# Kernel tuning notes

Hardware: AMD Instinct MI355X
Metric: run time of the kernel (lower is better)

## Reference

```python
import jax, jax.numpy as jnp
import numpy as np

B, P_DIM, H_DIM, X_DIM = 4096, 1024, 2048, 1024


def setup_inputs() -> dict:
    key = jax.random.key(0)
    ks = jax.random.split(key, 24)
    def lin_w(k, out_d, in_d):
        bound = 1.0 / np.sqrt(in_d)
        return jax.random.uniform(k, (out_d, in_d), jnp.float32, -bound, bound)
    def lin_b(k, out_d, in_d):
        bound = 1.0 / np.sqrt(in_d)
        return jax.random.uniform(k, (out_d,), jnp.float32, -bound, bound)
    inp = {
        "P": jax.random.normal(ks[0], (B, P_DIM), jnp.float32),
        "hidden": jax.random.normal(ks[1], (B, H_DIM), jnp.float32),
        "cell": jax.random.normal(ks[2], (B, H_DIM), jnp.float32),
        "ext_input": jax.random.normal(ks[3], (B, X_DIM), jnp.float32),
        "W_pi": lin_w(ks[4], H_DIM, P_DIM), "b_pi": lin_b(ks[5], H_DIM, P_DIM),
        "W_pf": lin_w(ks[6], H_DIM, P_DIM), "b_pf": lin_b(ks[7], H_DIM, P_DIM),
        "W_pg": lin_w(ks[8], H_DIM, P_DIM), "b_pg": lin_b(ks[9], H_DIM, P_DIM),
        "W_po": lin_w(ks[10], H_DIM, P_DIM), "b_po": lin_b(ks[11], H_DIM, P_DIM),
        "W_hi": lin_w(ks[12], H_DIM, H_DIM), "W_hf": lin_w(ks[13], H_DIM, H_DIM),
        "W_hg": lin_w(ks[14], H_DIM, H_DIM), "W_ho": lin_w(ks[15], H_DIM, H_DIM),
        "W_xi": lin_w(ks[16], H_DIM, X_DIM), "W_xf": lin_w(ks[17], H_DIM, X_DIM),
        "W_xg": lin_w(ks[18], H_DIM, X_DIM), "W_xo": lin_w(ks[19], H_DIM, X_DIM),
    }
    return inp


def reference(P, hidden, cell, ext_input,
              W_pi, b_pi, W_pf, b_pf, W_pg, b_pg, W_po, b_po,
              W_hi, W_hf, W_hg, W_ho,
              W_xi, W_xf, W_xg, W_xo):
    # Concatenate the 4 per-gate weights along the output axis -> 3 big GEMMs
    # (mathematically identical to the 12 separate nn.Linear calls).
    Wp = jnp.concatenate([W_pi, W_pf, W_pg, W_po], axis=0)   # [4H, P]
    bp = jnp.concatenate([b_pi, b_pf, b_pg, b_po], axis=0)   # [4H]
    Wh = jnp.concatenate([W_hi, W_hf, W_hg, W_ho], axis=0)   # [4H, H]
    Wx = jnp.concatenate([W_xi, W_xf, W_xg, W_xo], axis=0)   # [4H, X]
    gates = P @ Wp.T + bp + hidden @ Wh.T + ext_input @ Wx.T  # [B, 4H]
    gi, gf, gg, go = jnp.split(gates, 4, axis=-1)
    i = jax.nn.sigmoid(gi)
    f = jax.nn.sigmoid(gf)
    g = jnp.tanh(gg)
    o = jax.nn.sigmoid(go)
    c_new = f * cell + i * g
    h_new = o * jnp.tanh(c_new)
    return (h_new, c_new)
```

## Files before the change

kernel.cpp:

```cpp
#include <hip/hip_runtime.h>
#include <hip/hip_bf16.h>
#include <stdint.h>

#define B_DIM 4096
#define P_DIMC 1024
#define H_DIMC 2048
#define X_DIMC 1024
#define K_DIM 4096
#define N_DIM 8192

#define BM 256
#define BN 256
#define BK 32
#define NT (K_DIM / BK)

typedef __attribute__((ext_vector_type(8))) short bf16x8;
typedef __attribute__((ext_vector_type(4))) float f32x4;

template <int V> struct Int { static constexpr int value = V; };

__device__ __forceinline__ unsigned short f2bf(float f) {
  union { float f; unsigned u; } v; v.f = f;
  unsigned u = v.u;
  u += 0x7FFFu + ((u >> 16) & 1u);
  return (unsigned short)(u >> 16);
}

__device__ __forceinline__ float sigm(float x) { return 1.f / (1.f + __expf(-x)); }
__device__ __forceinline__ float tanh_fast(float x) {
  float e = __expf(2.f * x);
  return 1.f - 2.f / (e + 1.f);
}

__device__ __forceinline__ void gl_lds16(const void* g, void* l) {
  __builtin_amdgcn_global_load_lds((const __attribute__((address_space(1))) void*)g,
                                   (__attribute__((address_space(3))) void*)l, 16, 0, 0);
}

__global__ void pack_a_kernel(const float* __restrict__ P, const float* __restrict__ Hd,
                              const float* __restrict__ X, unsigned short* __restrict__ A) {
  const int total = B_DIM * (K_DIM / 4);
  for (int idx = blockIdx.x * blockDim.x + threadIdx.x; idx < total;
       idx += gridDim.x * blockDim.x) {
    int row = idx >> 10;
    int col = (idx & 1023) << 2;
    const float* src; int off;
    if (col < P_DIMC)                { src = P;  off = row * P_DIMC + col; }
    else if (col < P_DIMC + H_DIMC)  { src = Hd; off = row * H_DIMC + (col - P_DIMC); }
    else                             { src = X;  off = row * X_DIMC + (col - P_DIMC - H_DIMC); }
    float4 v = *(const float4*)(src + off);
    ushort4 o;
    o.x = f2bf(v.x); o.y = f2bf(v.y); o.z = f2bf(v.z); o.w = f2bf(v.w);
    *(ushort4*)(A + (size_t)row * K_DIM + col) = o;
  }
}

struct WPtrs {
  const float *pi, *pf, *pg, *po;
  const float *hi, *hf, *hg, *ho;
  const float *xi, *xf, *xg, *xo;
};

__global__ void pack_w_kernel(WPtrs w, unsigned short* __restrict__ Wo) {
  const int total = N_DIM * (K_DIM / 4);
  for (int idx = blockIdx.x * blockDim.x + threadIdx.x; idx < total;
       idx += gridDim.x * blockDim.x) {
    int n = idx >> 10;
    int col = (idx & 1023) << 2;
    int gate = (n >> 4) & 3;
    int h = ((n >> 6) << 4) | (n & 15);
    const float* src; int off;
    if (col < P_DIMC) {
      src = gate == 0 ? w.pi : gate == 1 ? w.pf : gate == 2 ? w.pg : w.po;
      off = h * P_DIMC + col;
    } else if (col < P_DIMC + H_DIMC) {
      src = gate == 0 ? w.hi : gate == 1 ? w.hf : gate == 2 ? w.hg : w.ho;
      off = h * H_DIMC + (col - P_DIMC);
    } else {
      src = gate == 0 ? w.xi : gate == 1 ? w.xf : gate == 2 ? w.xg : w.xo;
      off = h * X_DIMC + (col - P_DIMC - H_DIMC);
    }
    float4 v = *(const float4*)(src + off);
    ushort4 o;
    o.x = f2bf(v.x); o.y = f2bf(v.y); o.z = f2bf(v.z); o.w = f2bf(v.w);
    *(ushort4*)(Wo + (size_t)n * K_DIM + col) = o;
  }
}

__global__ __launch_bounds__(512, 1) void gemm_lstm_kernel(
    const unsigned short* __restrict__ A, const unsigned short* __restrict__ W,
    const float* __restrict__ cell,
    const float* __restrict__ bpi, const float* __restrict__ bpf,
    const float* __restrict__ bpg, const float* __restrict__ bpo,
    float* __restrict__ out) {
  __shared__ __align__(16) short As[4][BM * BK];
  __shared__ __align__(16) short Bs[4][BN * BK];

  const int T = threadIdx.x;
  const int wave = T >> 6, lane = T & 63;
  const int wm = wave >> 2, wn = wave & 3;

  const int x = blockIdx.x & 7, local = blockIdx.x >> 3;
  const int bm = (x & 1) * 8 + (local >> 3);
  const int bn = (x >> 1) * 8 + (local & 7);

  const int cg = ((T & 3) - (T >> 3)) & 3;
  const int rowS = T >> 2;
  const unsigned short* aG0 = A + (size_t)(bm * BM + rowS) * K_DIM + cg * 8;
  const unsigned short* aG1 = A + (size_t)(bm * BM + 128 + rowS) * K_DIM + cg * 8;
  const unsigned short* bG0 = W + (size_t)(bn * BN + rowS) * K_DIM + cg * 8;
  const unsigned short* bG1 = W + (size_t)(bn * BN + 128 + rowS) * K_DIM + cg * 8;
  const int dstOff = T * 8;

  const int lrow = lane & 15, kgrp = lane >> 4;
  const int slotR = (kgrp + (lrow >> 1)) & 3;
  int offA[8], offB[4];
#pragma unroll
  for (int mf = 0; mf < 8; ++mf) offA[mf] = (wm * 128 + mf * 16 + lrow) * BK + slotR * 8;
#pragma unroll
  for (int nf = 0; nf < 4; ++nf) offB[nf] = (wn * 64 + nf * 16 + lrow) * BK + slotR * 8;

  f32x4 acc[8][4] = {};

#pragma unroll
  for (int u = 0; u < 3; ++u) {
    short* dA = &As[u][0];
    short* dB = &Bs[u][0];
    const int kt = u * BK;
    gl_lds16(aG0 + kt, dA + dstOff);
    gl_lds16(aG1 + kt, dA + 4096 + dstOff);
    gl_lds16(bG0 + kt, dB + dstOff);
    gl_lds16(bG1 + kt, dB + 4096 + dstOff);
  }
  asm volatile("s_waitcnt vmcnt(8)" ::: "memory");
  __builtin_amdgcn_s_barrier();

  auto run_loop = [&](auto firstc) {
    constexpr int FIRST = decltype(firstc)::value;
    constexpr int SECOND = 4 - FIRST;
    for (int t = 0; t < NT; ++t) {
      const short* bufA = &As[t & 3][0];
      const short* bufB = &Bs[t & 3][0];
      const int kt = (t + 3) * BK;
      short* dA = &As[(t + 3) & 3][0];
      short* dB = &Bs[(t + 3) & 3][0];
      bf16x8 av[4], bv[4];

#pragma unroll
      for (int i = 0; i < 4; ++i) bv[i] = *(const bf16x8*)(bufB + offB[i]);
#pragma unroll
      for (int i = 0; i < 4; ++i) av[i] = *(const bf16x8*)(bufA + offA[FIRST + i]);
      if (t < NT - 3) {
        gl_lds16(aG0 + kt, dA + dstOff);
        gl_lds16(aG1 + kt, dA + 4096 + dstOff);
      }
      __builtin_amdgcn_s_setprio(1);
#pragma unroll
      for (int mi = 0; mi < 4; ++mi)
#pragma unroll
        for (int ni = 0; ni < 4; ++ni)
          acc[FIRST + mi][ni] =
              __builtin_amdgcn_mfma_f32_16x16x32_bf16(av[mi], bv[ni], acc[FIRST + mi][ni], 0, 0, 0);
      __builtin_amdgcn_s_setprio(0);
      __builtin_amdgcn_sched_barrier(0);

#pragma unroll
      for (int i = 0; i < 4; ++i) av[i] = *(const bf16x8*)(bufA + offA[SECOND + i]);
      if (t < NT - 3) {
        gl_lds16(bG0 + kt, dB + dstOff);
        gl_lds16(bG1 + kt, dB + 4096 + dstOff);
      }
      __builtin_amdgcn_s_setprio(1);
#pragma unroll
      for (int mi = 0; mi < 4; ++mi)
#pragma unroll
        for (int ni = 0; ni < 4; ++ni)
          acc[SECOND + mi][ni] =
              __builtin_amdgcn_mfma_f32_16x16x32_bf16(av[mi], bv[ni], acc[SECOND + mi][ni], 0, 0, 0);
      __builtin_amdgcn_s_setprio(0);
      __builtin_amdgcn_sched_barrier(0);

      if (t < NT - 3)       { asm volatile("s_waitcnt vmcnt(8)" ::: "memory"); }
      else if (t == NT - 3) { asm volatile("s_waitcnt vmcnt(4)" ::: "memory"); }
      else if (t == NT - 2) { asm volatile("s_waitcnt vmcnt(0)" ::: "memory"); }
      __builtin_amdgcn_s_barrier();
    }
  };
  if (wave & 1) run_loop(Int<4>{});
  else          run_loop(Int<0>{});

  const int h = bn * 64 + wn * 16 + lrow;
  const float bi = bpi[h], bf_ = bpf[h], bg = bpg[h], bo = bpo[h];
  const int rbase = bm * BM + wm * 128 + kgrp * 4;
#pragma unroll
  for (int mf = 0; mf < 8; ++mf) {
#pragma unroll
    for (int r = 0; r < 4; ++r) {
      const int brow = rbase + mf * 16 + r;
      float gi = acc[mf][0][r] + bi;
      float gf = acc[mf][1][r] + bf_;
      float gg = acc[mf][2][r] + bg;
      float go = acc[mf][3][r] + bo;
      float i_ = sigm(gi), f_ = sigm(gf), g_ = tanh_fast(gg), o_ = sigm(go);
      float cold = cell[(size_t)brow * H_DIMC + h];
      float cn = f_ * cold + i_ * g_;
      out[(size_t)brow * H_DIMC + h] = o_ * tanh_fast(cn);
      out[(size_t)B_DIM * H_DIMC + (size_t)brow * H_DIMC + h] = cn;
    }
  }
}

extern "C" void kernel_launch(void* const* d_in, const int* in_sizes, int n_in,
                              void* d_out, int out_size, void* d_ws, size_t ws_size,
                              hipStream_t stream) {
  const float* P    = (const float*)d_in[0];
  const float* Hd   = (const float*)d_in[1];
  const float* cell = (const float*)d_in[2];
  const float* X    = (const float*)d_in[3];
  WPtrs w;
  w.pi = (const float*)d_in[4];   const float* bpi = (const float*)d_in[5];
  w.pf = (const float*)d_in[6];   const float* bpf = (const float*)d_in[7];
  w.pg = (const float*)d_in[8];   const float* bpg = (const float*)d_in[9];
  w.po = (const float*)d_in[10];  const float* bpo = (const float*)d_in[11];
  w.hi = (const float*)d_in[12];  w.hf = (const float*)d_in[13];
  w.hg = (const float*)d_in[14];  w.ho = (const float*)d_in[15];
  w.xi = (const float*)d_in[16];  w.xf = (const float*)d_in[17];
  w.xg = (const float*)d_in[18];  w.xo = (const float*)d_in[19];

  unsigned short* Abf = (unsigned short*)d_ws;
  unsigned short* Wbf = Abf + (size_t)B_DIM * K_DIM;

  pack_a_kernel<<<2048, 256, 0, stream>>>(P, Hd, X, Abf);
  pack_w_kernel<<<2048, 256, 0, stream>>>(w, Wbf);
  gemm_lstm_kernel<<<512, 512, 0, stream>>>(Abf, Wbf, cell, bpi, bpf, bpg, bpo,
                                            (float*)d_out);
}
```

Measured before the change: 300.5 us.

## Switch GEMM to 32x32x16 MFMA tiles with 4x2 wave layout and 32-wide gate interleave

Replaces the 16x16x32 bf16 MFMA with the 32x32x16 variant. Each wave now computes a 64x128 sub-tile in a 4x2 wave grid, and the packed weight layout interleaves gates in groups of 32 columns so that each lane still holds all four gates for its hidden unit. The larger MFMA shape needs fewer LDS fragment reads per FLOP and fewer MFMA issues, which should raise tensor-core throughput. LDS read addressing and the epilogue row mapping change to match the 32x32 accumulator layout, so a mistake in that mapping could give wrong results.

```diff
diff --git a/kernel.cpp b/kernel.cpp
--- a/kernel.cpp
+++ b/kernel.cpp
@@ -15,7 +15,7 @@
 #define NT (K_DIM / BK)
 
 typedef __attribute__((ext_vector_type(8))) short bf16x8;
-typedef __attribute__((ext_vector_type(4))) float f32x4;
+typedef __attribute__((ext_vector_type(16))) float f32x16;
 
 template <int V> struct Int { static constexpr int value = V; };
 
@@ -67,8 +67,8 @@
        idx += gridDim.x * blockDim.x) {
     int n = idx >> 10;
     int col = (idx & 1023) << 2;
-    int gate = (n >> 4) & 3;
-    int h = ((n >> 6) << 4) | (n & 15);
+    int gate = (n >> 5) & 3;
+    int h = (n >> 7) * 32 + (n & 31);
     const float* src; int off;
     if (col < P_DIMC) {
       src = gate == 0 ? w.pi : gate == 1 ? w.pf : gate == 2 ? w.pg : w.po;
@@ -98,7 +98,7 @@
 
   const int T = threadIdx.x;
   const int wave = T >> 6, lane = T & 63;
-  const int wm = wave >> 2, wn = wave & 3;
+  const int wm = wave >> 1, wn = wave & 1;
 
   const int x = blockIdx.x & 7, local = blockIdx.x >> 3;
   const int bm = (x & 1) * 8 + (local >> 3);
@@ -112,15 +112,22 @@
   const unsigned short* bG1 = W + (size_t)(bn * BN + 128 + rowS) * K_DIM + cg * 8;
   const int dstOff = T * 8;
 
-  const int lrow = lane & 15, kgrp = lane >> 4;
-  const int slotR = (kgrp + (lrow >> 1)) & 3;
-  int offA[8], offB[4];
-#pragma unroll
-  for (int mf = 0; mf < 8; ++mf) offA[mf] = (wm * 128 + mf * 16 + lrow) * BK + slotR * 8;
-#pragma unroll
-  for (int nf = 0; nf < 4; ++nf) offB[nf] = (wn * 64 + nf * 16 + lrow) * BK + slotR * 8;
-
-  f32x4 acc[8][4] = {};
+  const int l31 = lane & 31, khalf = lane >> 5;
+  int offA[2][2], offB[4][2];
+#pragma unroll
+  for (int mf = 0; mf < 2; ++mf)
+#pragma unroll
+    for (int ks = 0; ks < 2; ++ks)
+      offA[mf][ks] = (wm * 64 + mf * 32 + l31) * BK +
+                     (((ks * 2 + khalf) + (l31 >> 1)) & 3) * 8;
+#pragma unroll
+  for (int nf = 0; nf < 4; ++nf)
+#pragma unroll
+    for (int ks = 0; ks < 2; ++ks)
+      offB[nf][ks] = (wn * 128 + nf * 32 + l31) * BK +
+                     (((ks * 2 + khalf) + (l31 >> 1)) & 3) * 8;
+
+  f32x16 acc[2][4] = {};
 
 #pragma unroll
   for (int u = 0; u < 3; ++u) {
@@ -135,48 +142,50 @@
   asm volatile("s_waitcnt vmcnt(8)" ::: "memory");
   __builtin_amdgcn_s_barrier();
 
-  auto run_loop = [&](auto firstc) {
-    constexpr int FIRST = decltype(firstc)::value;
-    constexpr int SECOND = 4 - FIRST;
+  auto run_loop = [&](auto kfc) {
+    constexpr int KF = decltype(kfc)::value;
+    constexpr int KS = 1 - KF;
     for (int t = 0; t < NT; ++t) {
       const short* bufA = &As[t & 3][0];
       const short* bufB = &Bs[t & 3][0];
       const int kt = (t + 3) * BK;
       short* dA = &As[(t + 3) & 3][0];
       short* dB = &Bs[(t + 3) & 3][0];
-      bf16x8 av[4], bv[4];
-
-#pragma unroll
-      for (int i = 0; i < 4; ++i) bv[i] = *(const bf16x8*)(bufB + offB[i]);
-#pragma unroll
-      for (int i = 0; i < 4; ++i) av[i] = *(const bf16x8*)(bufA + offA[FIRST + i]);
+      bf16x8 av[2], bv[4];
+
+#pragma unroll
+      for (int i = 0; i < 2; ++i) av[i] = *(const bf16x8*)(bufA + offA[i][KF]);
+#pragma unroll
+      for (int j = 0; j < 4; ++j) bv[j] = *(const bf16x8*)(bufB + offB[j][KF]);
       if (t < NT - 3) {
         gl_lds16(aG0 + kt, dA + dstOff);
         gl_lds16(aG1 + kt, dA + 4096 + dstOff);
       }
       __builtin_amdgcn_s_setprio(1);
 #pragma unroll
-      for (int mi = 0; mi < 4; ++mi)
+      for (int mi = 0; mi < 2; ++mi)
 #pragma unroll
         for (int ni = 0; ni < 4; ++ni)
-          acc[FIRST + mi][ni] =
-              __builtin_amdgcn_mfma_f32_16x16x32_bf16(av[mi], bv[ni], acc[FIRST + mi][ni], 0, 0, 0);
+          acc[mi][ni] =
+              __builtin_amdgcn_mfma_f32_32x32x16_bf16(av[mi], bv[ni], acc[mi][ni], 0, 0, 0);
       __builtin_amdgcn_s_setprio(0);
       __builtin_amdgcn_sched_barrier(0);
 
 #pragma unroll
-      for (int i = 0; i < 4; ++i) av[i] = *(const bf16x8*)(bufA + offA[SECOND + i]);
+      for (int i = 0; i < 2; ++i) av[i] = *(const bf16x8*)(bufA + offA[i][KS]);
+#pragma unroll
+      for (int j = 0; j < 4; ++j) bv[j] = *(const bf16x8*)(bufB + offB[j][KS]);
       if (t < NT - 3) {
         gl_lds16(bG0 + kt, dB + dstOff);
         gl_lds16(bG1 + kt, dB + 4096 + dstOff);
       }
       __builtin_amdgcn_s_setprio(1);
 #pragma unroll
-      for (int mi = 0; mi < 4; ++mi)
+      for (int mi = 0; mi < 2; ++mi)
 #pragma unroll
         for (int ni = 0; ni < 4; ++ni)
-          acc[SECOND + mi][ni] =
-              __builtin_amdgcn_mfma_f32_16x16x32_bf16(av[mi], bv[ni], acc[SECOND + mi][ni], 0, 0, 0);
+          acc[mi][ni] =
+              __builtin_amdgcn_mfma_f32_32x32x16_bf16(av[mi], bv[ni], acc[mi][ni], 0, 0, 0);
       __builtin_amdgcn_s_setprio(0);
       __builtin_amdgcn_sched_barrier(0);
 
@@ -186,21 +195,21 @@
       __builtin_amdgcn_s_barrier();
     }
   };
-  if (wave & 1) run_loop(Int<4>{});
+  if (wave & 1) run_loop(Int<1>{});
   else          run_loop(Int<0>{});
 
-  const int h = bn * 64 + wn * 16 + lrow;
+  const int h = bn * 64 + wn * 32 + l31;
   const float bi = bpi[h], bf_ = bpf[h], bg = bpg[h], bo = bpo[h];
-  const int rbase = bm * BM + wm * 128 + kgrp * 4;
-#pragma unroll
-  for (int mf = 0; mf < 8; ++mf) {
-#pragma unroll
-    for (int r = 0; r < 4; ++r) {
-      const int brow = rbase + mf * 16 + r;
-      float gi = acc[mf][0][r] + bi;
-      float gf = acc[mf][1][r] + bf_;
-      float gg = acc[mf][2][r] + bg;
-      float go = acc[mf][3][r] + bo;
+  const int rbase = bm * BM + wm * 64 + khalf * 4;
+#pragma unroll
+  for (int mf = 0; mf < 2; ++mf) {
+#pragma unroll
+    for (int reg = 0; reg < 16; ++reg) {
+      const int brow = rbase + mf * 32 + (reg & 3) + 8 * (reg >> 2);
+      float gi = acc[mf][0][reg] + bi;
+      float gf = acc[mf][1][reg] + bf_;
+      float gg = acc[mf][2][reg] + bg;
+      float go = acc[mf][3][reg] + bo;
       float i_ = sigm(gi), f_ = sigm(gf), g_ = tanh_fast(gg), o_ = sigm(go);
       float cold = cell[(size_t)brow * H_DIMC + h];
       float cn = f_ * cold + i_ * g_;
```

Result: slower. 333.0 us (+10.8%).
